# Performance work log

Measured on AMD Instinct MI355X. Metric: run time of the kernel, lower is better.

Reference implementation:

```python
import jax, jax.numpy as jnp
import numpy as np

APERTURE = 128
LN_EPS = 1e-6

def _layer_norm(y, g, b):
    mu = jnp.mean(y, axis=-1, keepdims=True)
    var = jnp.var(y, axis=-1, keepdims=True)
    return (y - mu) / jnp.sqrt(var + LN_EPS) * g + b

def setup_inputs() -> dict:
    key = jax.random.key(0)
    ks = jax.random.split(key, 12)
    B, S, D = 4, 4096, 1024
    gain = np.sqrt(2.0)
    xav = lambda k, fan_out, fan_in: jax.random.uniform(
        k, (fan_out, fan_in), jnp.float32,
        -gain * np.sqrt(6.0 / (fan_in + fan_out)), gain * np.sqrt(6.0 / (fan_in + fan_out)))
    return {
        "x": jax.random.normal(ks[0], (B, S, D), jnp.float32),
        "Wq": xav(ks[1], D, D),
        "Wk": xav(ks[2], D, D),
        "Wv": xav(ks[3], D, D),
        "Wo": xav(ks[4], D, D),
        "k1_w": xav(ks[5], D, D),
        "k1_b": jnp.full((D,), 0.1, jnp.float32),
        "k2_w": xav(ks[6], 1, D),
        "k2_b": jnp.full((1,), 0.1, jnp.float32),
        "ln_g": jnp.ones((D,), jnp.float32),
        "ln_b": jnp.zeros((D,), jnp.float32),
    }

def reference(x, Wq, Wk, Wv, Wo, k1_w, k1_b, k2_w, k2_b, ln_g, ln_b):
    B, S, D = x.shape
    scale = jnp.float32(1.0 / np.sqrt(D))
    neg_inf = jnp.float32(-np.inf)

    Q = x @ Wq.T  # [B,S,D]
    K = x @ Wk.T
    V = x @ Wv.T

    e = jnp.einsum('bsd,btd->bst', Q, K) * scale  # [B,S,S]

    # ignore_self: -inf on the diagonal
    i = jnp.arange(S)[:, None]
    j = jnp.arange(S)[None, :]
    e = jnp.where(i == j, neg_inf, e)

    # banded aperture mask: tril(e, ap) * triu(e, -ap); zeros of the product -> -inf
    d = j - i
    scope = jnp.where(d <= APERTURE, e, 0.0) * jnp.where(d >= -APERTURE, e, 0.0)
    e = jnp.where(scope == 0.0, neg_inf, e)

    alpha = jax.nn.softmax(e, axis=2)
    c = jnp.einsum('bst,btd->bsd', alpha, V)
    c = c @ Wo.T

    y = c + x
    y = _layer_norm(y, ln_g, ln_b)
    y = jax.nn.relu(y @ k1_w.T + k1_b)
    y = _layer_norm(y, ln_g, ln_b)
    y = jax.nn.sigmoid(y @ k2_w.T + k2_b)  # [B,S,1]
    return y.reshape(B, S)
```

## Files before the change

### kernel.cpp

```cpp
#include <hip/hip_runtime.h>
#include <math.h>

#define DD 1024
#define SS 4096
#define AP 128
#define LN_EPS 1e-6f
#define BK 32
#define BAND 384

typedef __bf16 bf16;
typedef __attribute__((ext_vector_type(4))) __bf16 bf16x4;
typedef __attribute__((ext_vector_type(8))) __bf16 bf16x8;
typedef __attribute__((ext_vector_type(4))) float f32x4;

#define GLOAD_LDS16(g, l)                                                   \
    __builtin_amdgcn_global_load_lds(                                        \
        (const __attribute__((address_space(1))) void*)(g),                  \
        (__attribute__((address_space(3))) void*)(l), 16, 0, 0)

__global__ __launch_bounds__(256) void prep_all(const float* __restrict__ x,
                                                const float* __restrict__ Wq,
                                                const float* __restrict__ Wk,
                                                const float* __restrict__ Wv,
                                                const float* __restrict__ Wo,
                                                const float* __restrict__ k1w,
                                                const float* __restrict__ k1b,
                                                const float* __restrict__ lng,
                                                const float* __restrict__ lnb,
                                                bf16* __restrict__ xb,
                                                bf16* __restrict__ Wob,
                                                bf16* __restrict__ k1g,
                                                bf16* __restrict__ Wtb,
                                                float* __restrict__ u1,
                                                float* __restrict__ c1b) {
    __shared__ float tile[64][65];
    const int bid = blockIdx.x;
    const int tid = threadIdx.x;
    if (bid < 16384) {
        const int i = (bid * 256 + tid) * 4;
        const float4 a = *(const float4*)(x + i);
        bf16x4 o;
        o[0] = (__bf16)a.x; o[1] = (__bf16)a.y; o[2] = (__bf16)a.z; o[3] = (__bf16)a.w;
        *(bf16x4*)(xb + i) = o;
        return;
    }
    if (bid < 18432) {
        const int b2 = bid - 16384;
        const int sel = b2 >> 10;
        const int bb = b2 & 1023;
        const float* s = sel ? k1w : Wo;
        bf16* d = sel ? k1g : Wob;
        const int i = (bb * 256 + tid) * 4;
        float4 a = *(const float4*)(s + i);
        if (sel) {
            const float4 g4 = *(const float4*)(lng + (i & (DD - 1)));
            a.x *= g4.x; a.y *= g4.y; a.z *= g4.z; a.w *= g4.w;
        }
        bf16x4 o;
        o[0] = (__bf16)a.x; o[1] = (__bf16)a.y; o[2] = (__bf16)a.z; o[3] = (__bf16)a.w;
        *(bf16x4*)(d + i) = o;
        return;
    }
    if (bid < 19200) {
        const int t = bid - 18432;
        const int tz = t >> 8;
        const int tb_ = t & 255;
        const float* in = (tz == 0) ? Wq : (tz == 1) ? Wk : Wv;
        bf16* out = Wtb + ((size_t)tz << 20);
        const int r0 = (tb_ >> 4) * 64, c0 = (tb_ & 15) * 64;
        const int lr = tid >> 4;
        const int lc = (tid & 15) * 4;
#pragma unroll
        for (int rr = 0; rr < 4; rr++) {
            const int row = lr + rr * 16;
            const float4 v = *(const float4*)(in + (size_t)(r0 + row) * DD + c0 + lc);
            tile[row][lc] = v.x; tile[row][lc + 1] = v.y;
            tile[row][lc + 2] = v.z; tile[row][lc + 3] = v.w;
        }
        __syncthreads();
#pragma unroll
        for (int rr = 0; rr < 4; rr++) {
            const int row = lr + rr * 16;
            bf16x4 o;
            o[0] = (__bf16)tile[lc + 0][row];
            o[1] = (__bf16)tile[lc + 1][row];
            o[2] = (__bf16)tile[lc + 2][row];
            o[3] = (__bf16)tile[lc + 3][row];
            *(bf16x4*)(out + (size_t)(c0 + row) * DD + r0 + lc) = o;
        }
        return;
    }
    const int pv = bid - 19200;
    const int lane = tid & 63, wave = tid >> 6;
    const int n = pv * 4 + wave;
    const float* row = k1w + (size_t)n * DD + lane * 16;
    float su = 0.f, sb = 0.f;
#pragma unroll
    for (int q = 0; q < 4; q++) {
        const float4 a = *(const float4*)(row + q * 4);
        const float4 g4 = *(const float4*)(lng + lane * 16 + q * 4);
        const float4 b4 = *(const float4*)(lnb + lane * 16 + q * 4);
        su += a.x * g4.x + a.y * g4.y + a.z * g4.z + a.w * g4.w;
        sb += a.x * b4.x + a.y * b4.y + a.z * b4.z + a.w * b4.w;
    }
#pragma unroll
    for (int off = 32; off > 0; off >>= 1) {
        su += __shfl_xor(su, off);
        sb += __shfl_xor(sb, off);
    }
    if (lane == 0) {
        u1[n] = su;
        c1b[n] = sb + k1b[n];
    }
}

__global__ __launch_bounds__(256) void gemm_pair(const bf16* __restrict__ A0,
                                                 const bf16* __restrict__ W0,
                                                 bf16* __restrict__ O0,
                                                 const bf16* __restrict__ A1,
                                                 const bf16* __restrict__ W1,
                                                 bf16* __restrict__ O1) {
    const bf16* A = blockIdx.z ? A1 : A0;
    const bf16* W = blockIdx.z ? W1 : W0;
    bf16* O = blockIdx.z ? O1 : O0;
    __shared__ bf16 As[128 * BK];
    __shared__ bf16 Bs[128 * BK];
    const int tid = threadIdx.x;
    const int lane = tid & 63;
    const int wave = tid >> 6;
    const int wm = wave & 1;
    const int wn = wave >> 1;
    const int m0 = blockIdx.y * 128;
    const int n0 = blockIdx.x * 128;

    const int c = wave * 64 + lane;
    const int ar = c >> 2;
    const int ac = (c & 3) << 3;
    char* AsB = (char*)As;
    char* BsB = (char*)Bs;
    const int lr = lane & 15;
    const int lk = (lane >> 4) << 3;

    f32x4 acc[4][4] = {};

    for (int kt = 0; kt < DD; kt += BK) {
        const bf16* ga0 = A + (size_t)(m0 + ar) * DD + kt + ac;
        const bf16* gb0 = W + (size_t)(n0 + ar) * DD + kt + ac;
        GLOAD_LDS16(ga0, AsB + wave * 1024);
        GLOAD_LDS16(ga0 + (size_t)64 * DD, AsB + 4096 + wave * 1024);
        GLOAD_LDS16(gb0, BsB + wave * 1024);
        GLOAD_LDS16(gb0 + (size_t)64 * DD, BsB + 4096 + wave * 1024);
        __syncthreads();

        bf16x8 af[4], bfr[4];
#pragma unroll
        for (int i = 0; i < 4; i++)
            af[i] = *(const bf16x8*)&As[(wm * 64 + i * 16 + lr) * BK + lk];
#pragma unroll
        for (int j = 0; j < 4; j++)
            bfr[j] = *(const bf16x8*)&Bs[(wn * 64 + j * 16 + lr) * BK + lk];
#pragma unroll
        for (int i = 0; i < 4; i++)
#pragma unroll
            for (int j = 0; j < 4; j++)
                acc[i][j] = __builtin_amdgcn_mfma_f32_16x16x32_bf16(af[i], bfr[j], acc[i][j], 0, 0, 0);
        __syncthreads();
    }

#pragma unroll
    for (int i = 0; i < 4; i++) {
        const int row = m0 + wm * 64 + i * 16 + ((lane >> 4) << 2);
#pragma unroll
        for (int j = 0; j < 4; j++) {
            const int col = n0 + wn * 64 + j * 16 + (lane & 15);
#pragma unroll
            for (int rr = 0; rr < 4; rr++)
                O[(size_t)(row + rr) * DD + col] = (__bf16)acc[i][j][rr];
        }
    }
}


#define KL_STAGE_A(tt, hh, bb)                                               \
    {                                                                        \
        const bf16* gp_ = Aop + gofsA + (tt) * 64 + (hh) * 32;               \
        GLOAD_LDS16(gp_, smem + (bb) + (hh) * 16384 + ldsW);                 \
        GLOAD_LDS16(gp_ + (size_t)128 * DD,                                  \
                    smem + (bb) + (hh) * 16384 + 8192 + ldsW);               \
    }
#define KL_STAGE_B(tt, hh, bb)                                               \
    {                                                                        \
        const bf16* gp_ = Bop + gofsB + (tt) * 64 + (hh) * 32;               \
        GLOAD_LDS16(gp_, smem + (bb) + 32768 + (hh) * 16384 + ldsW);         \
        GLOAD_LDS16(gp_ + (size_t)128 * DD,                                  \
                    smem + (bb) + 32768 + (hh) * 16384 + 8192 + ldsW);       \
    }
#define KL_READS_A(ks, mh)                                                   \
    af[0] = *(const bf16x8*)(sA + bufo + (ks) * 16384 + (mh) * 4096);        \
    af[1] = *(const bf16x8*)(sA + bufo + (ks) * 16384 + (mh) * 4096 + 1024); \
    af[2] = *(const bf16x8*)(sA + bufo + (ks) * 16384 + (mh) * 4096 + 2048); \
    af[3] = *(const bf16x8*)(sA + bufo + (ks) * 16384 + (mh) * 4096 + 3072);
#define KL_READS_B(ks)                                                       \
    bfr[0] = *(const bf16x8*)(sB + bufo + (ks) * 16384);                     \
    bfr[1] = *(const bf16x8*)(sB + bufo + (ks) * 16384 + 1024);              \
    bfr[2] = *(const bf16x8*)(sB + bufo + (ks) * 16384 + 2048);              \
    bfr[3] = *(const bf16x8*)(sB + bufo + (ks) * 16384 + 3072);
#define KL_MFMA4(I, MH)                                                      \
    acc[(MH) * 4 + I][0] = __builtin_amdgcn_mfma_f32_16x16x32_bf16(af[I], bfr[0], acc[(MH) * 4 + I][0], 0, 0, 0); \
    acc[(MH) * 4 + I][1] = __builtin_amdgcn_mfma_f32_16x16x32_bf16(af[I], bfr[1], acc[(MH) * 4 + I][1], 0, 0, 0); \
    acc[(MH) * 4 + I][2] = __builtin_amdgcn_mfma_f32_16x16x32_bf16(af[I], bfr[2], acc[(MH) * 4 + I][2], 0, 0, 0); \
    acc[(MH) * 4 + I][3] = __builtin_amdgcn_mfma_f32_16x16x32_bf16(af[I], bfr[3], acc[(MH) * 4 + I][3], 0, 0, 0);
#define KL_MFMA16(MH)                                                        \
    __builtin_amdgcn_s_setprio(1);                                           \
    KL_MFMA4(0, MH) KL_MFMA4(1, MH) KL_MFMA4(2, MH) KL_MFMA4(3, MH)          \
    __builtin_amdgcn_s_setprio(0);
#define KL_BARRIER(N) asm volatile("s_waitcnt vmcnt(" #N ")\n\ts_barrier" ::: "memory")

__device__ __forceinline__ void kloop256(const bf16* __restrict__ Aop,
                                         const bf16* __restrict__ Bop,
                                         const int m0, const int n0,
                                         char* smem, f32x4 (&acc)[8][4],
                                         const int tid, const int lane,
                                         const int wave, const int wm, const int wn) {
    const int grow = tid >> 2;
    const int gslot = (tid & 3) ^ ((tid >> 3) & 3);
    const size_t gofsA = (size_t)(m0 + grow) * DD + gslot * 8;
    const size_t gofsB = (size_t)(n0 + grow) * DD + gslot * 8;
    const int ldsW = wave * 1024;
    const int sxo = (((lane >> 4) ^ ((lane >> 1) & 3)) << 4);
    const char* sA = smem + wm * 8192 + (lane & 15) * 64 + sxo;
    const char* sB = smem + 32768 + wn * 4096 + (lane & 15) * 64 + sxo;

    bf16x8 af[4], bfr[4];

    KL_STAGE_A(0, 0, 0) KL_STAGE_B(0, 0, 0)
    KL_STAGE_A(0, 1, 0) KL_STAGE_B(0, 1, 0)
    KL_STAGE_A(1, 0, 65536) KL_STAGE_B(1, 0, 65536)

    int bufo = 0;
    for (int t = 0; t < 15; t++) {
        const int nb = bufo ^ 65536;
        KL_BARRIER(8);
        KL_READS_A(0, 0) KL_READS_B(0)
        KL_STAGE_A(t + 1, 1, nb)
        KL_MFMA16(0)
        KL_READS_A(0, 1)
        KL_STAGE_B(t + 1, 1, nb)
        KL_MFMA16(1)
        KL_BARRIER(8);
        KL_READS_A(1, 0) KL_READS_B(1)
        if (t < 14) { KL_STAGE_A(t + 2, 0, bufo) }
        KL_MFMA16(0)
        KL_READS_A(1, 1)
        if (t < 14) { KL_STAGE_B(t + 2, 0, bufo) }
        KL_MFMA16(1)
        bufo = nb;
    }
    KL_BARRIER(4);
    KL_READS_A(0, 0) KL_READS_B(0)
    KL_MFMA16(0)
    KL_READS_A(0, 1)
    KL_MFMA16(1)
    KL_BARRIER(0);
    KL_READS_A(1, 0) KL_READS_B(1)
    KL_MFMA16(0)
    KL_READS_A(1, 1)
    KL_MFMA16(1)
}

__global__ __launch_bounds__(512) void gemm_uv(const bf16* __restrict__ xb,
                                               const bf16* __restrict__ Gt,
                                               const bf16* __restrict__ W2,
                                               bf16* __restrict__ Ub,
                                               bf16* __restrict__ Vt2) {
    __shared__ char smem[131072];
    const int s = blockIdx.x;
    const int half = s >> 8;
    const int sh = s & 255;
    const int p = (sh & 7) | ((sh >> 5) << 3);
    const int q = (sh >> 3) & 3;
    const bf16* A;
    const bf16* W;
    bf16* O;
    int m0, n0;
    size_t ldo;
    if (half == 0) {
        A = xb; W = Gt; O = Ub;
        m0 = p * 256; n0 = q * 256; ldo = DD;
    } else {
        A = W2; W = xb; O = Vt2;
        m0 = q * 256; n0 = p * 256; ldo = (size_t)4 * SS;
    }
    const int tid = threadIdx.x;
    const int lane = tid & 63;
    const int wave = tid >> 6;
    const int wm = wave & 1;
    const int wn = wave >> 1;

    f32x4 acc[8][4] = {};
    kloop256(A, W, m0, n0, smem, acc, tid, lane, wave, wm, wn);

#pragma unroll
    for (int a = 0; a < 8; a++) {
        const int row = m0 + wm * 128 + a * 16 + ((lane >> 4) << 2);
#pragma unroll
        for (int j = 0; j < 4; j++) {
            const int col = n0 + wn * 64 + j * 16 + (lane & 15);
#pragma unroll
            for (int rr = 0; rr < 4; rr++)
                O[(size_t)(row + rr) * ldo + col] = (__bf16)acc[a][j][rr];
        }
    }
}

__global__ __launch_bounds__(512) void gemm_k1(const bf16* __restrict__ T,
                                               const bf16* __restrict__ k1g,
                                               const float* __restrict__ part_t,
                                               const float* __restrict__ u1,
                                               const float* __restrict__ c1b,
                                               const float* __restrict__ lng,
                                               const float* __restrict__ k2w,
                                               float* __restrict__ part_h) {
    __shared__ char smem[131072];
    __shared__ float lmu[256], lrs[256];
    const int m0 = blockIdx.x * 256;
    const int n0 = blockIdx.y * 256;
    const int tid = threadIdx.x;
    const int lane = tid & 63;
    const int wave = tid >> 6;
    const int wm = wave & 1;
    const int wn = wave >> 1;

    if (tid < 256) {
        const float* p = part_t + (size_t)(m0 + tid) * 32;
        float s1 = 0.f, s2 = 0.f;
#pragma unroll
        for (int s = 0; s < 8; s++) {
            const float4 v = *(const float4*)(p + s * 4);
            s1 += v.x + v.z;
            s2 += v.y + v.w;
        }
        const float m = s1 * (1.f / DD);
        lmu[tid] = m;
        lrs[tid] = rsqrtf(s2 * (1.f / DD) - m * m + LN_EPS);
    }
    __syncthreads();

    f32x4 acc[8][4] = {};
    kloop256(T, k1g, m0, n0, smem, acc, tid, lane, wave, wm, wn);

    float u1v[4], cbv[4], ugv[4];
#pragma unroll
    for (int j = 0; j < 4; j++) {
        const int col = n0 + wn * 64 + j * 16 + (lane & 15);
        u1v[j] = u1[col];
        cbv[j] = c1b[col];
        ugv[j] = lng[col] * k2w[col];
    }
    const int strip = blockIdx.y * 4 + wn;
#pragma unroll
    for (int a = 0; a < 8; a++) {
#pragma unroll
        for (int rr = 0; rr < 4; rr++) {
            const int lrow = wm * 128 + a * 16 + ((lane >> 4) << 2) + rr;
            const int row = m0 + lrow;
            const float mr = lmu[lrow], rs = lrs[lrow];
            float s1 = 0.f, s2 = 0.f, s3 = 0.f;
#pragma unroll
            for (int j = 0; j < 4; j++) {
                const float v = rs * (acc[a][j][rr] - mr * u1v[j]) + cbv[j];
                const float h = fmaxf(v, 0.f);
                s1 += h; s2 += h * h; s3 += h * ugv[j];
            }
#pragma unroll
            for (int off = 8; off > 0; off >>= 1) {
                s1 += __shfl_xor(s1, off);
                s2 += __shfl_xor(s2, off);
                s3 += __shfl_xor(s3, off);
            }
            if ((lane & 15) == 0) {
                float* p = part_h + (size_t)row * 48 + strip * 3;
                p[0] = s1; p[1] = s2; p[2] = s3;
            }
        }
    }
}

__global__ __launch_bounds__(256) void attn_s_mfma(const bf16* __restrict__ U,
                                                   const bf16* __restrict__ X,
                                                   float* __restrict__ S) {
    __shared__ bf16 As[128 * BK];
    __shared__ bf16 Bs[128 * BK];
    const int tid = threadIdx.x;
    const int lane = tid & 63;
    const int wave = tid >> 6;
    const int wm = wave & 1;
    const int wn = wave >> 1;
    const int t = blockIdx.x;
    const int nb = blockIdx.y;
    const int m0 = t * 128;
    const long w0 = (long)t * 128 - 128 + (long)nb * 128;

    const int c = wave * 64 + lane;
    const int ar = c >> 2;
    const int ac = (c & 3) << 3;
    char* AsB = (char*)As;
    char* BsB = (char*)Bs;
    const int lr = lane & 15;
    const int lk = (lane >> 4) << 3;

    f32x4 acc[4][4] = {};

    for (int kt = 0; kt < DD; kt += BK) {
        const bf16* ga0 = U + (size_t)(m0 + ar) * DD + kt + ac;
        const bf16* gb0 = X + (w0 + ar) * DD + kt + ac;
        GLOAD_LDS16(ga0, AsB + wave * 1024);
        GLOAD_LDS16(ga0 + (size_t)64 * DD, AsB + 4096 + wave * 1024);
        GLOAD_LDS16(gb0, BsB + wave * 1024);
        GLOAD_LDS16(gb0 + (size_t)64 * DD, BsB + 4096 + wave * 1024);
        __syncthreads();

        bf16x8 af[4], bfr[4];
#pragma unroll
        for (int i = 0; i < 4; i++)
            af[i] = *(const bf16x8*)&As[(wm * 64 + i * 16 + lr) * BK + lk];
#pragma unroll
        for (int j = 0; j < 4; j++)
            bfr[j] = *(const bf16x8*)&Bs[(wn * 64 + j * 16 + lr) * BK + lk];
#pragma unroll
        for (int i = 0; i < 4; i++)
#pragma unroll
            for (int j = 0; j < 4; j++)
                acc[i][j] = __builtin_amdgcn_mfma_f32_16x16x32_bf16(af[i], bfr[j], acc[i][j], 0, 0, 0);
        __syncthreads();
    }

#pragma unroll
    for (int i = 0; i < 4; i++) {
        const int row = m0 + wm * 64 + i * 16 + ((lane >> 4) << 2);
#pragma unroll
        for (int j = 0; j < 4; j++) {
            const int col = nb * 128 + wn * 64 + j * 16 + (lane & 15);
#pragma unroll
            for (int rr = 0; rr < 4; rr++)
                S[(size_t)(row + rr) * BAND + col] = acc[i][j][rr];
        }
    }
}

__global__ __launch_bounds__(256) void attn_softmax(const float* __restrict__ S,
                                                    bf16* __restrict__ P) {
    const int wave = threadIdx.x >> 6;
    const int lane = threadIdx.x & 63;
    const int g = blockIdx.x * 4 + wave;
    const int i = g & (SS - 1);
    const int j_start = ((i >> 7) << 7) - 128;
    const float scale = 0.03125f;
    float s[6];
    float m = -INFINITY;
#pragma unroll
    for (int t = 0; t < 6; t++) {
        const int jj = lane + t * 64;
        const int j = j_start + jj;
        const int dj = j - i;
        const bool valid = (j >= 0) && (j < SS) && (dj != 0) && (dj <= AP) && (dj >= -AP);
        const float v = S[(size_t)g * BAND + jj] * scale;
        s[t] = valid ? v : -INFINITY;
        m = fmaxf(m, s[t]);
    }
#pragma unroll
    for (int off = 32; off > 0; off >>= 1) m = fmaxf(m, __shfl_xor(m, off));
    float l = 0.f;
#pragma unroll
    for (int t = 0; t < 6; t++) {
        s[t] = __expf(s[t] - m);
        l += s[t];
    }
#pragma unroll
    for (int off = 32; off > 0; off >>= 1) l += __shfl_xor(l, off);
    const float inv = 1.f / l;
#pragma unroll
    for (int t = 0; t < 6; t++)
        P[(size_t)g * BAND + lane + t * 64] = (__bf16)(s[t] * inv);
}

__global__ __launch_bounds__(512) void attn_pv_mfma(const bf16* __restrict__ P,
                                                    const bf16* __restrict__ Vt,
                                                    const bf16* __restrict__ xres,
                                                    bf16* __restrict__ T,
                                                    float* __restrict__ part_t) {
    __shared__ bf16 As[128 * BK];
    __shared__ bf16 Bs[256 * BK];
    const int tid = threadIdx.x;
    const int lane = tid & 63;
    const int wave = tid >> 6;
    const int wm = wave & 1;
    const int wn = wave >> 1;
    const int t = blockIdx.x;
    const int m0 = t * 128;
    const int n0 = blockIdx.y * 256;
    const bf16* Wb = Vt + (long)t * 128 - 128;

    const int ar = tid >> 2;
    const int ac = (tid & 3) << 3;
    char* AsB = (char*)As;
    char* BsB = (char*)Bs;
    const int lr = lane & 15;
    const int lk = (lane >> 4) << 3;

    f32x4 acc[4][4] = {};

    for (int kt = 0; kt < BAND; kt += BK) {
        const bf16* ga0 = P + (size_t)(m0 + ar) * BAND + kt + ac;
        const bf16* gb0 = Wb + (size_t)(n0 + ar) * (4 * SS) + kt + ac;
        GLOAD_LDS16(ga0, AsB + wave * 1024);
        GLOAD_LDS16(gb0, BsB + wave * 1024);
        GLOAD_LDS16(gb0 + (size_t)128 * (4 * SS), BsB + 8192 + wave * 1024);
        __syncthreads();

        bf16x8 af[4], bfr[4];
#pragma unroll
        for (int i = 0; i < 4; i++)
            af[i] = *(const bf16x8*)&As[(wm * 64 + i * 16 + lr) * BK + lk];
#pragma unroll
        for (int j = 0; j < 4; j++)
            bfr[j] = *(const bf16x8*)&Bs[(wn * 64 + j * 16 + lr) * BK + lk];
#pragma unroll
        for (int i = 0; i < 4; i++)
#pragma unroll
            for (int j = 0; j < 4; j++)
                acc[i][j] = __builtin_amdgcn_mfma_f32_16x16x32_bf16(af[i], bfr[j], acc[i][j], 0, 0, 0);
        __syncthreads();
    }

    const int strip = blockIdx.y * 4 + wn;
#pragma unroll
    for (int i = 0; i < 4; i++) {
#pragma unroll
        for (int rr = 0; rr < 4; rr++) {
            const int row = m0 + wm * 64 + i * 16 + ((lane >> 4) << 2) + rr;
            float s1 = 0.f, s2 = 0.f;
#pragma unroll
            for (int j = 0; j < 4; j++) {
                const int col = n0 + wn * 64 + j * 16 + (lane & 15);
                const size_t idx = (size_t)row * DD + col;
                const __bf16 tv_b = (__bf16)(acc[i][j][rr] + (float)xres[idx]);
                T[idx] = tv_b;
                const float tv = (float)tv_b;
                s1 += tv; s2 += tv * tv;
            }
#pragma unroll
            for (int off = 8; off > 0; off >>= 1) {
                s1 += __shfl_xor(s1, off);
                s2 += __shfl_xor(s2, off);
            }
            if ((lane & 15) == 0) {
                float2 st; st.x = s1; st.y = s2;
                *(float2*)(part_t + (size_t)row * 32 + strip * 2) = st;
            }
        }
    }
}

__global__ __launch_bounds__(256) void ln_k2_p(const float* __restrict__ part_h,
                                               const float* __restrict__ g,
                                               const float* __restrict__ bta,
                                               const float* __restrict__ w2,
                                               const float* __restrict__ b2,
                                               float* __restrict__ out) {
    __shared__ float red[256], red2[256];
    const int tid = threadIdx.x;
    const float4 g4 = *(const float4*)(g + tid * 4);
    const float4 w4 = *(const float4*)(w2 + tid * 4);
    const float4 b4 = *(const float4*)(bta + tid * 4);
    red[tid] = g4.x * w4.x + g4.y * w4.y + g4.z * w4.z + g4.w * w4.w;
    red2[tid] = b4.x * w4.x + b4.y * w4.y + b4.z * w4.z + b4.w * w4.w;
    __syncthreads();
    for (int s = 128; s > 0; s >>= 1) {
        if (tid < s) { red[tid] += red[tid + s]; red2[tid] += red2[tid + s]; }
        __syncthreads();
    }
    const float sum_u = red[0];
    const float sum_bw = red2[0];

    const int r = blockIdx.x * 256 + tid;
    const float* p = part_h + (size_t)r * 48;
    float s1 = 0.f, s2 = 0.f, s3 = 0.f;
#pragma unroll
    for (int s = 0; s < 16; s++) {
        s1 += p[s * 3 + 0];
        s2 += p[s * 3 + 1];
        s3 += p[s * 3 + 2];
    }
    const float m = s1 * (1.f / DD);
    const float var = s2 * (1.f / DD) - m * m;
    const float rs = rsqrtf(var + LN_EPS);
    const float z = rs * (s3 - m * sum_u) + sum_bw + b2[0];
    out[r] = 1.f / (1.f + __expf(-z));
}

extern "C" void kernel_launch(void* const* d_in, const int* in_sizes, int n_in,
                              void* d_out, int out_size, void* d_ws, size_t ws_size,
                              hipStream_t stream) {
    const float* x   = (const float*)d_in[0];
    const float* Wq  = (const float*)d_in[1];
    const float* Wk  = (const float*)d_in[2];
    const float* Wv  = (const float*)d_in[3];
    const float* Wo  = (const float*)d_in[4];
    const float* k1w = (const float*)d_in[5];
    const float* k1b = (const float*)d_in[6];
    const float* k2w = (const float*)d_in[7];
    const float* k2b = (const float*)d_in[8];
    const float* lng = (const float*)d_in[9];
    const float* lnb = (const float*)d_in[10];
    float* out = (float*)d_out;

    const int N = 4 * SS;
    char* ws = (char*)d_ws;
    bf16*  Ub   = (bf16*)(ws);
    bf16*  xb   = (bf16*)(ws + ((size_t)32  << 20));
    bf16*  Vt2  = (bf16*)(ws + ((size_t)64  << 20));
    bf16*  P    = (bf16*)(ws + ((size_t)96  << 20));
    float* S    = (float*)(ws + ((size_t)108 << 20));
    bf16*  T    = (bf16*)(ws + ((size_t)164 << 20));
    bf16*  Wtb  = (bf16*)(ws + ((size_t)196 << 20));
    bf16*  Wqtb = Wtb;
    bf16*  Wktb = Wqtb + (1 << 20);
    bf16*  Wvtb = Wktb + (1 << 20);
    bf16*  Wob  = Wvtb + (1 << 20);
    bf16*  k1g  = Wob  + (1 << 20);
    bf16*  Gtb  = k1g  + (1 << 20);
    bf16*  W2b  = Gtb  + (1 << 20);
    float* u1     = (float*)(ws + ((size_t)210 << 20));
    float* c1b    = u1 + DD;
    float* part_t = (float*)(ws + ((size_t)211 << 20));
    float* part_h = (float*)(ws + ((size_t)214 << 20));

    dim3 tb(256);

    prep_all<<<19456, tb, 0, stream>>>(x, Wq, Wk, Wv, Wo, k1w, k1b, lng, lnb,
                                       xb, Wob, k1g, Wtb, u1, c1b);

    gemm_pair<<<dim3(8, 8, 2), tb, 0, stream>>>(Wktb, Wqtb, Gtb, Wob, Wvtb, W2b);

    gemm_uv<<<512, dim3(512), 0, stream>>>(xb, Gtb, W2b, Ub, Vt2);

    attn_s_mfma<<<dim3(N / 128, 3), tb, 0, stream>>>(Ub, xb, S);
    attn_softmax<<<N / 4, tb, 0, stream>>>(S, P);
    attn_pv_mfma<<<dim3(N / 128, 4), dim3(512), 0, stream>>>(P, Vt2, xb, T, part_t);

    gemm_k1<<<dim3(64, 4), dim3(512), 0, stream>>>(T, k1g, part_t, u1, c1b, lng, k2w, part_h);
    ln_k2_p<<<N / 256, tb, 0, stream>>>(part_h, lng, lnb, k2w, k2b, out);
}
```

Measured before the change: 333.9 us.

## Fuse banded score GEMM with softmax into one kernel writing bf16 probabilities

After: 335.6 us. No clear change (+0.5%).

```diff
diff --git a/kernel.cpp b/kernel.cpp
--- a/kernel.cpp
+++ b/kernel.cpp
@@ -386,102 +386,129 @@
     }
 }
 
-__global__ __launch_bounds__(256) void attn_s_mfma(const bf16* __restrict__ U,
-                                                   const bf16* __restrict__ X,
-                                                   float* __restrict__ S) {
-    __shared__ bf16 As[128 * BK];
-    __shared__ bf16 Bs[128 * BK];
+__global__ __launch_bounds__(512) void attn_sp(const bf16* __restrict__ U,
+                                               const bf16* __restrict__ X,
+                                               bf16* __restrict__ P) {
+    __shared__ bf16 As[64 * BK];
+    __shared__ bf16 Bs[384 * BK];
+    const int s = blockIdx.x;
+    const int t = (s & 7) * 32 + ((s >> 3) >> 1) * 2 + ((s >> 3) & 1);
     const int tid = threadIdx.x;
     const int lane = tid & 63;
     const int wave = tid >> 6;
     const int wm = wave & 1;
     const int wn = wave >> 1;
-    const int t = blockIdx.x;
-    const int nb = blockIdx.y;
-    const int m0 = t * 128;
-    const long w0 = (long)t * 128 - 128 + (long)nb * 128;
-
-    const int c = wave * 64 + lane;
-    const int ar = c >> 2;
-    const int ac = (c & 3) << 3;
-    char* AsB = (char*)As;
-    char* BsB = (char*)Bs;
-    const int lr = lane & 15;
-    const int lk = (lane >> 4) << 3;
-
-    f32x4 acc[4][4] = {};
+    const int m0 = t * 64;
+    const long w0 = (long)(t >> 1) * 128 - 128;
+
+    const int grow = tid >> 2;
+    const int gslot = (tid & 3) ^ ((tid >> 3) & 3);
+    const size_t gofsA = (size_t)(m0 + (grow & 63)) * DD + gslot * 8;
+    const long gofsB = (w0 + grow) * (long)DD + gslot * 8;
+    const int ldsW = wave * 1024;
+    const int sxo = (((lane >> 4) ^ ((lane >> 1) & 3)) << 4);
+    const char* sA = (const char*)As + (lane & 15) * 64 + sxo;
+    const char* sB = (const char*)Bs + (lane & 15) * 64 + sxo;
+
+    f32x4 acc[2][6] = {};
 
     for (int kt = 0; kt < DD; kt += BK) {
-        const bf16* ga0 = U + (size_t)(m0 + ar) * DD + kt + ac;
-        const bf16* gb0 = X + (w0 + ar) * DD + kt + ac;
-        GLOAD_LDS16(ga0, AsB + wave * 1024);
-        GLOAD_LDS16(ga0 + (size_t)64 * DD, AsB + 4096 + wave * 1024);
-        GLOAD_LDS16(gb0, BsB + wave * 1024);
-        GLOAD_LDS16(gb0 + (size_t)64 * DD, BsB + 4096 + wave * 1024);
-        __syncthreads();
-
-        bf16x8 af[4], bfr[4];
-#pragma unroll
-        for (int i = 0; i < 4; i++)
-            af[i] = *(const bf16x8*)&As[(wm * 64 + i * 16 + lr) * BK + lk];
-#pragma unroll
-        for (int j = 0; j < 4; j++)
-            bfr[j] = *(const bf16x8*)&Bs[(wn * 64 + j * 16 + lr) * BK + lk];
-#pragma unroll
-        for (int i = 0; i < 4; i++)
-#pragma unroll
-            for (int j = 0; j < 4; j++)
+        if (wave < 4) { GLOAD_LDS16(U + gofsA + kt, (char*)As + ldsW); }
+        GLOAD_LDS16(X + gofsB + kt, (char*)Bs + ldsW);
+        GLOAD_LDS16(X + gofsB + (long)128 * DD + kt, (char*)Bs + 8192 + ldsW);
+        GLOAD_LDS16(X + gofsB + (long)256 * DD + kt, (char*)Bs + 16384 + ldsW);
+        __syncthreads();
+
+        bf16x8 af[2], bfr[6];
+#pragma unroll
+        for (int i = 0; i < 2; i++)
+            af[i] = *(const bf16x8*)(sA + wm * 2048 + i * 1024);
+#pragma unroll
+        for (int j = 0; j < 6; j++)
+            bfr[j] = *(const bf16x8*)(sB + wn * 6144 + j * 1024);
+#pragma unroll
+        for (int i = 0; i < 2; i++)
+#pragma unroll
+            for (int j = 0; j < 6; j++)
                 acc[i][j] = __builtin_amdgcn_mfma_f32_16x16x32_bf16(af[i], bfr[j], acc[i][j], 0, 0, 0);
         __syncthreads();
     }
 
-#pragma unroll
-    for (int i = 0; i < 4; i++) {
-        const int row = m0 + wm * 64 + i * 16 + ((lane >> 4) << 2);
-#pragma unroll
-        for (int j = 0; j < 4; j++) {
-            const int col = nb * 128 + wn * 64 + j * 16 + (lane & 15);
+    float* lredm = (float*)As;
+    float* lreds = lredm + 256;
+    const int rbase = wm * 32 + ((lane >> 4) << 2);
+    const int ib = (t << 6) & (SS - 1);
+    const int jst = ((t >> 1) & 31) * 128 - 128;
+    const float scale = 0.03125f;
+
+    float pmx[2][4];
+#pragma unroll
+    for (int i = 0; i < 2; i++)
+#pragma unroll
+        for (int rr = 0; rr < 4; rr++) {
+            const int irow = ib + rbase + i * 16 + rr;
+            float mx = -INFINITY;
+#pragma unroll
+            for (int j = 0; j < 6; j++) {
+                const int jg = jst + wn * 96 + j * 16 + (lane & 15);
+                const int dj = jg - irow;
+                const bool valid = (jg >= 0) && (jg < SS) && (dj != 0) && (dj <= AP) && (dj >= -AP);
+                const float sv = valid ? acc[i][j][rr] * scale : -INFINITY;
+                acc[i][j][rr] = sv;
+                mx = fmaxf(mx, sv);
+            }
+#pragma unroll
+            for (int off = 8; off > 0; off >>= 1) mx = fmaxf(mx, __shfl_xor(mx, off));
+            pmx[i][rr] = mx;
+        }
+    if ((lane & 15) == 0) {
+#pragma unroll
+        for (int i = 0; i < 2; i++)
 #pragma unroll
             for (int rr = 0; rr < 4; rr++)
-                S[(size_t)(row + rr) * BAND + col] = acc[i][j][rr];
-        }
-    }
-}
-
-__global__ __launch_bounds__(256) void attn_softmax(const float* __restrict__ S,
-                                                    bf16* __restrict__ P) {
-    const int wave = threadIdx.x >> 6;
-    const int lane = threadIdx.x & 63;
-    const int g = blockIdx.x * 4 + wave;
-    const int i = g & (SS - 1);
-    const int j_start = ((i >> 7) << 7) - 128;
-    const float scale = 0.03125f;
-    float s[6];
-    float m = -INFINITY;
-#pragma unroll
-    for (int t = 0; t < 6; t++) {
-        const int jj = lane + t * 64;
-        const int j = j_start + jj;
-        const int dj = j - i;
-        const bool valid = (j >= 0) && (j < SS) && (dj != 0) && (dj <= AP) && (dj >= -AP);
-        const float v = S[(size_t)g * BAND + jj] * scale;
-        s[t] = valid ? v : -INFINITY;
-        m = fmaxf(m, s[t]);
-    }
-#pragma unroll
-    for (int off = 32; off > 0; off >>= 1) m = fmaxf(m, __shfl_xor(m, off));
-    float l = 0.f;
-#pragma unroll
-    for (int t = 0; t < 6; t++) {
-        s[t] = __expf(s[t] - m);
-        l += s[t];
-    }
-#pragma unroll
-    for (int off = 32; off > 0; off >>= 1) l += __shfl_xor(l, off);
-    const float inv = 1.f / l;
-#pragma unroll
-    for (int t = 0; t < 6; t++)
-        P[(size_t)g * BAND + lane + t * 64] = (__bf16)(s[t] * inv);
+                lredm[(rbase + i * 16 + rr) * 4 + wn] = pmx[i][rr];
+    }
+    __syncthreads();
+
+    float lsum[2][4], mv[2][4];
+#pragma unroll
+    for (int i = 0; i < 2; i++)
+#pragma unroll
+        for (int rr = 0; rr < 4; rr++) {
+            const int ri = (rbase + i * 16 + rr) * 4;
+            mv[i][rr] = fmaxf(fmaxf(lredm[ri], lredm[ri + 1]),
+                              fmaxf(lredm[ri + 2], lredm[ri + 3]));
+            float su = 0.f;
+#pragma unroll
+            for (int j = 0; j < 6; j++) {
+                const float e = __expf(acc[i][j][rr] - mv[i][rr]);
+                acc[i][j][rr] = e;
+                su += e;
+            }
+#pragma unroll
+            for (int off = 8; off > 0; off >>= 1) su += __shfl_xor(su, off);
+            lsum[i][rr] = su;
+        }
+    if ((lane & 15) == 0) {
+#pragma unroll
+        for (int i = 0; i < 2; i++)
+#pragma unroll
+            for (int rr = 0; rr < 4; rr++)
+                lreds[(rbase + i * 16 + rr) * 4 + wn] = lsum[i][rr];
+    }
+    __syncthreads();
+
+#pragma unroll
+    for (int i = 0; i < 2; i++)
+#pragma unroll
+        for (int rr = 0; rr < 4; rr++) {
+            const int ri = (rbase + i * 16 + rr) * 4;
+            const float inv = 1.f / (lreds[ri] + lreds[ri + 1] + lreds[ri + 2] + lreds[ri + 3]);
+            const size_t ro = (size_t)(m0 + rbase + i * 16 + rr) * BAND;
+#pragma unroll
+            for (int j = 0; j < 6; j++)
+                P[ro + wn * 96 + j * 16 + (lane & 15)] = (__bf16)(acc[i][j][rr] * inv);
+        }
 }
 
 __global__ __launch_bounds__(512) void attn_pv_mfma(const bf16* __restrict__ P,
@@ -621,7 +648,6 @@
     bf16*  xb   = (bf16*)(ws + ((size_t)32  << 20));
     bf16*  Vt2  = (bf16*)(ws + ((size_t)64  << 20));
     bf16*  P    = (bf16*)(ws + ((size_t)96  << 20));
-    float* S    = (float*)(ws + ((size_t)108 << 20));
     bf16*  T    = (bf16*)(ws + ((size_t)164 << 20));
     bf16*  Wtb  = (bf16*)(ws + ((size_t)196 << 20));
     bf16*  Wqtb = Wtb;
@@ -645,8 +671,7 @@
 
     gemm_uv<<<512, dim3(512), 0, stream>>>(xb, Gtb, W2b, Ub, Vt2);
 
-    attn_s_mfma<<<dim3(N / 128, 3), tb, 0, stream>>>(Ub, xb, S);
-    attn_softmax<<<N / 4, tb, 0, stream>>>(S, P);
+    attn_sp<<<256, dim3(512), 0, stream>>>(Ub, xb, P);
     attn_pv_mfma<<<dim3(N / 128, 4), dim3(512), 0, stream>>>(P, Vt2, xb, T, part_t);
 
     gemm_k1<<<dim3(64, 4), dim3(512), 0, stream>>>(T, k1g, part_t, u1, c1b, lng, k2w, part_h);
```
